# Optimization experiments

Hardware: AMD Instinct MI355X
Metric: run time of the kernel (lower is better)

Reference implementation:

```python
import jax, jax.numpy as jnp
import numpy as np

EMB_DIM = 1024
NUM_HEADS = 16
HEAD_DIM = EMB_DIM // NUM_HEADS
B, S = 4, 1024


def _split_heads(x):
    # [B, S, E] -> [B, H, S, E/H]
    b, s, e = x.shape
    return x.reshape(b, s, NUM_HEADS, e // NUM_HEADS).transpose(0, 2, 1, 3)


def _merge_heads(x):
    # [B, H, S, D] -> [B, S, H*D]
    b, h, s, d = x.shape
    return x.transpose(0, 2, 1, 3).reshape(b, s, h * d)


def setup_inputs() -> dict:
    key = jax.random.key(0)
    ks = jax.random.split(key, 8)
    w_scale = 0.02
    return {
        "Re": jax.random.normal(ks[0], (B, S, EMB_DIM), jnp.float32),
        "Im": jax.random.normal(ks[1], (B, S, EMB_DIM), jnp.float32),
        "pos_enc": jax.random.normal(ks[2], (B, S, HEAD_DIM), jnp.float32),
        "Wq": jax.random.normal(ks[3], (EMB_DIM, EMB_DIM), jnp.float32) * w_scale,
        "bq": jnp.zeros((EMB_DIM,), jnp.float32),
        "Wk": jax.random.normal(ks[4], (EMB_DIM, EMB_DIM), jnp.float32) * w_scale,
        "bk": jnp.zeros((EMB_DIM,), jnp.float32),
        "Wv": jax.random.normal(ks[5], (EMB_DIM, EMB_DIM), jnp.float32) * w_scale,
        "bv": jnp.zeros((EMB_DIM,), jnp.float32),
        "Wo": jax.random.normal(ks[6], (EMB_DIM, EMB_DIM), jnp.float32) * w_scale,
        "bo": jnp.zeros((EMB_DIM,), jnp.float32),
    }


def reference(Re, Im, pos_enc, Wq, bq, Wk, bk, Wv, bv, Wo, bo):
    # projections + head split
    Q = _split_heads(Re @ Wq + bq)          # [B,H,S,D]
    K = _split_heads(Re @ Wk + bk)          # [B,H,S,D]
    ImH = _split_heads(Im)                  # [B,H,S,D]
    P = pos_enc[:, None, :, :]              # [B,1,S,D] broadcast over heads
    Q = Q + P
    K = K + P
    # real part of (Q + i*Im)(K - i*Im)^T = Q K^T + Im Im^T
    denom = jnp.sqrt(jnp.asarray(EMB_DIM, Q.dtype))  # NOTE: sqrt(emb_dim), as in source
    scores = (jnp.einsum("bhqd,bhkd->bhqk", Q, K)
              + jnp.einsum("bhqd,bhkd->bhqk", ImH, ImH)) / denom
    weights = jax.nn.softmax(scores, axis=-1)
    V = _split_heads(Re @ Wv + bv) + P      # value_pos_enc=True
    out = jnp.einsum("bhqk,bhkd->bhqd", weights, V)
    return _merge_heads(out) @ Wo + bo
```

## Files before the change

kernel.cpp:

```cpp
#include <hip/hip_runtime.h>
#include <hip/hip_bf16.h>
#include <stdint.h>

#define BATCH 4
#define SEQ   1024
#define EMB   1024
#define NHEAD 16
#define HDIM  64
#define MTOT  (BATCH*SEQ)
#define MELEM (MTOT*EMB)

typedef __attribute__((ext_vector_type(8))) short short8;
typedef __attribute__((ext_vector_type(4))) float f32x4;
typedef __attribute__((ext_vector_type(16))) float f32x16;
typedef __attribute__((ext_vector_type(4))) unsigned short us4;
typedef __attribute__((ext_vector_type(2))) unsigned int u32x2;
typedef __attribute__((ext_vector_type(4))) unsigned int u32x4;

static __device__ __forceinline__ unsigned short f2bf_fast(float f) {
  unsigned u = __builtin_bit_cast(unsigned, f);
  return (unsigned short)((u + 0x8000u) >> 16);
}

static __device__ __forceinline__ unsigned cvt_pk_bf16(float lo, float hi) {
  unsigned r;
  asm("v_cvt_pk_bf16_f32 %0, %1, %2" : "=v"(r) : "v"(lo), "v"(hi));
  return r;
}

static __device__ __forceinline__ void cp16(const void* g, const void* lds_uniform) {
  __builtin_amdgcn_global_load_lds(
      (const __attribute__((address_space(1))) unsigned int*)(uintptr_t)g,
      (__attribute__((address_space(3))) unsigned int*)(unsigned int)(uintptr_t)lds_uniform,
      16, 0, 0);
}

__global__ __launch_bounds__(256) void cvt_bf16(const float* __restrict__ in0,
                                                const float* __restrict__ in1,
                                                short* __restrict__ out0,
                                                short* __restrict__ out1) {
  const float* in  = blockIdx.y ? in1  : in0;
  short*       out = blockIdx.y ? out1 : out0;
  int i = blockIdx.x * 256 + threadIdx.x;
  float4 f = ((const float4*)in)[i];
  unsigned r0 = ((unsigned)f2bf_fast(f.y) << 16) | f2bf_fast(f.x);
  unsigned r1 = ((unsigned)f2bf_fast(f.w) << 16) | f2bf_fast(f.z);
  ((uint2*)out)[i] = make_uint2(r0, r1);
}

__global__ __launch_bounds__(256) void wtrans(const float* __restrict__ W0,
                                              const float* __restrict__ W1,
                                              const float* __restrict__ W2,
                                              const float* __restrict__ W3,
                                              short* __restrict__ WtBase) {
  const int z = blockIdx.z;
  const float* W = (z == 0) ? W0 : (z == 1) ? W1 : (z == 2) ? W2 : W3;
  short* Wt = WtBase + (size_t)z * EMB * EMB;
  __shared__ short tile[32][33];
  int nT = blockIdx.x * 32, kT = blockIdx.y * 32;
  int tx = threadIdx.x, ty = threadIdx.y;
  #pragma unroll
  for (int i = 0; i < 4; ++i)
    tile[ty + 8*i][tx] = (short)f2bf_fast(W[(size_t)(kT + ty + 8*i) * EMB + nT + tx]);
  __syncthreads();
  #pragma unroll
  for (int i = 0; i < 4; ++i)
    Wt[(size_t)(nT + ty + 8*i) * EMB + kT + tx] = tile[tx][ty + 8*i];
}

__global__ __launch_bounds__(256) void gemm_qkv(const short* __restrict__ A,
                                                const short* __restrict__ Wt,
                                                const float* __restrict__ bq,
                                                const float* __restrict__ bk,
                                                const float* __restrict__ bv,
                                                const float* __restrict__ pos,
                                                short* __restrict__ QKbase,
                                                short* __restrict__ vtOut) {
  const int m0 = blockIdx.y * 128, n0 = blockIdx.x * 64;
  const int z = n0 >> 10;
  const float* bias = (z == 0) ? bq : (z == 1 ? bk : bv);

  __shared__ __align__(16) short As[128 * 64];
  __shared__ __align__(16) short Bs[64 * 64];

  const int t = threadIdx.x;
  const int lane = t & 63, w = t >> 6;
  const int wm = w >> 1, wn = w & 1;
  const int quad = lane >> 4, l16 = lane & 15;
  const int lrow8 = lane >> 3, lchunk = lane & 7;
  const int gch = lchunk ^ lrow8;
  const int sw7 = l16 & 7;

  const short* Arow = A  + (size_t)(m0 + w * 32 + lrow8) * EMB + gch * 8;
  const short* Brow = Wt + (size_t)(n0 + w * 16 + lrow8) * EMB + gch * 8;

  f32x4 acc[4][2] = {};

  for (int k0 = 0; k0 < EMB; k0 += 64) {
    #pragma unroll
    for (int s = 0; s < 4; ++s)
      cp16(Arow + (size_t)(s * 8) * EMB + k0, &As[(w * 32 + s * 8) * 64]);
    #pragma unroll
    for (int s = 0; s < 2; ++s)
      cp16(Brow + (size_t)(s * 8) * EMB + k0, &Bs[(w * 16 + s * 8) * 64]);
    __syncthreads();
    #pragma unroll
    for (int ks = 0; ks < 2; ++ks) {
      const int chv = ((ks << 2) + quad) ^ sw7;
      short8 af[4], bfr[2];
      #pragma unroll
      for (int i = 0; i < 4; ++i)
        af[i] = *(const short8*)&As[(wm * 64 + i * 16 + l16) * 64 + chv * 8];
      #pragma unroll
      for (int j = 0; j < 2; ++j)
        bfr[j] = *(const short8*)&Bs[(wn * 32 + j * 16 + l16) * 64 + chv * 8];
      #pragma unroll
      for (int i = 0; i < 4; ++i)
        #pragma unroll
        for (int j = 0; j < 2; ++j)
          acc[i][j] = __builtin_amdgcn_mfma_f32_16x16x32_bf16(af[i], bfr[j], acc[i][j], 0, 0, 0);
    }
    __syncthreads();
  }

  #pragma unroll
  for (int i = 0; i < 4; ++i) {
    int mbase = m0 + wm * 64 + i * 16 + quad * 4;
    #pragma unroll
    for (int j = 0; j < 2; ++j) {
      int n = n0 + wn * 32 + j * 16 + l16;
      int nl = n & 1023;
      float bn = bias[nl];
      int d = nl & (HDIM - 1);
      if (z == 2) {
        int bh = (mbase >> 10) * NHEAD + (nl >> 6);
        int s = mbase & (SEQ - 1);
        us4 pk;
        #pragma unroll
        for (int r = 0; r < 4; ++r) {
          float v = acc[i][j][r] + bn + pos[(size_t)(mbase + r) * HDIM + d];
          pk[r] = f2bf_fast(v);
        }
        *(us4*)&vtOut[((size_t)bh * HDIM + d) * SEQ + s] = pk;
      } else {
        #pragma unroll
        for (int r = 0; r < 4; ++r) {
          int mm = mbase + r;
          float v = acc[i][j][r] + bn + pos[(size_t)mm * HDIM + d];
          QKbase[(size_t)z * MELEM + (size_t)mm * EMB + nl] = (short)f2bf_fast(v);
        }
      }
    }
  }
}

__global__ __launch_bounds__(256) void gemm_wo(const short* __restrict__ A,
                                               const short* __restrict__ Bt,
                                               const float* __restrict__ bias,
                                               float* __restrict__ out) {
  const int m0 = blockIdx.y * 64, n0 = blockIdx.x * 64;

  __shared__ __align__(16) short As[64 * 64];
  __shared__ __align__(16) short Bs[64 * 64];

  const int t = threadIdx.x;
  const int lane = t & 63, w = t >> 6;
  const int wm = w >> 1, wn = w & 1;
  const int quad = lane >> 4, l16 = lane & 15;
  const int lrow8 = lane >> 3, lchunk = lane & 7;
  const int gch = lchunk ^ lrow8;
  const int sw7 = l16 & 7;

  const short* Arow = A  + (size_t)(m0 + w * 16 + lrow8) * EMB + gch * 8;
  const short* Brow = Bt + (size_t)(n0 + w * 16 + lrow8) * EMB + gch * 8;

  f32x4 acc[2][2] = {};

  for (int k0 = 0; k0 < EMB; k0 += 64) {
    #pragma unroll
    for (int s = 0; s < 2; ++s) {
      cp16(Arow + (size_t)(s * 8) * EMB + k0, &As[(w * 16 + s * 8) * 64]);
      cp16(Brow + (size_t)(s * 8) * EMB + k0, &Bs[(w * 16 + s * 8) * 64]);
    }
    __syncthreads();
    #pragma unroll
    for (int ks = 0; ks < 2; ++ks) {
      const int chv = ((ks << 2) + quad) ^ sw7;
      short8 af[2], bfr[2];
      #pragma unroll
      for (int i = 0; i < 2; ++i)
        af[i] = *(const short8*)&As[(wm * 32 + i * 16 + l16) * 64 + chv * 8];
      #pragma unroll
      for (int j = 0; j < 2; ++j)
        bfr[j] = *(const short8*)&Bs[(wn * 32 + j * 16 + l16) * 64 + chv * 8];
      #pragma unroll
      for (int i = 0; i < 2; ++i)
        #pragma unroll
        for (int j = 0; j < 2; ++j)
          acc[i][j] = __builtin_amdgcn_mfma_f32_16x16x32_bf16(af[i], bfr[j], acc[i][j], 0, 0, 0);
    }
    __syncthreads();
  }

  #pragma unroll
  for (int i = 0; i < 2; ++i) {
    int mbase = m0 + wm * 32 + i * 16 + quad * 4;
    #pragma unroll
    for (int j = 0; j < 2; ++j) {
      int n = n0 + wn * 32 + j * 16 + l16;
      float bn = bias[n];
      #pragma unroll
      for (int r = 0; r < 4; ++r)
        out[(size_t)(mbase + r) * EMB + n] = acc[i][j][r] + bn;
    }
  }
}

__global__ __launch_bounds__(256) void attn(const short* __restrict__ Qp,
                                            const short* __restrict__ Kp,
                                            const short* __restrict__ VtG,
                                            const short* __restrict__ Imb,
                                            short* __restrict__ attnA) {
  const int qb = blockIdx.y * 128;
  const int bh = blockIdx.x;
  const int b = bh >> 4, h = bh & 15;
  const int t = threadIdx.x, lane = t & 63, w = t >> 6;
  const int c31 = lane & 31;
  const int hi  = lane >> 5;
  const int lrow8 = lane >> 3, lchunk = lane & 7;
  const int gch = lchunk ^ lrow8;

  __shared__ __align__(16) short tiles[3 * 64 * 64];

  const int qrow = qb + w * 32 + c31;
  const size_t qbase = ((size_t)(b * SEQ + qrow)) * EMB + h * HDIM + hi * 8;
  short8 bq_[4], bim[4];
  #pragma unroll
  for (int ks = 0; ks < 4; ++ks) {
    bq_[ks] = *(const short8*)&Qp [qbase + ks * 16];
    bim[ks] = *(const short8*)&Imb[qbase + ks * 16];
  }

  float lrA = 0.f, lrB = 0.f;
  f32x16 o0 = {}, o1 = {};

  const float SC = 0.03125f * 1.44269504089f;
  const size_t kimBase = ((size_t)b * SEQ) * EMB + h * HDIM + gch * 8;
  const size_t vtBase  = ((size_t)bh * HDIM) * SEQ + gch * 8;

  #pragma unroll
  for (int s = 0; s < 6; ++s) {
    const int I = w * 6 + s;
    const int tz = I >> 3;
    const int row = ((I & 7) * 8) + lrow8;
    const short* g;
    if (tz == 0)      g = Kp  + kimBase + (size_t)row * EMB;
    else if (tz == 1) g = Imb + kimBase + (size_t)row * EMB;
    else              g = VtG + vtBase + (size_t)row * SEQ;
    cp16(g, &tiles[I * 512]);
  }
  __syncthreads();

  const int swz = c31 & 7;

  for (int kt = 0; kt < 16; ++kt) {
    const int kBaseN = (kt + 1) * 64;

    f32x16 s0 = {}, s1 = {};
    #pragma unroll
    for (int ks = 0; ks < 4; ++ks) {
      const int ch = ((ks * 2 + hi) ^ swz) * 8;
      const int r0off = c31 * 64 + ch, r1off = (32 + c31) * 64 + ch;
      short8 k0 = *(const short8*)&tiles[r0off];
      short8 k1 = *(const short8*)&tiles[r1off];
      short8 i0 = *(const short8*)&tiles[4096 + r0off];
      short8 i1 = *(const short8*)&tiles[4096 + r1off];
      s0 = __builtin_amdgcn_mfma_f32_32x32x16_bf16(k0, bq_[ks], s0, 0, 0, 0);
      s1 = __builtin_amdgcn_mfma_f32_32x32x16_bf16(k1, bq_[ks], s1, 0, 0, 0);
      s0 = __builtin_amdgcn_mfma_f32_32x32x16_bf16(i0, bim[ks], s0, 0, 0, 0);
      s1 = __builtin_amdgcn_mfma_f32_32x32x16_bf16(i1, bim[ks], s1, 0, 0, 0);
    }

    __syncthreads();

    if (kt != 15) {
      #pragma unroll
      for (int s = 0; s < 4; ++s) {
        const int I = w * 4 + s;
        const int row = ((I & 7) * 8) + lrow8;
        const short* g = ((I >> 3) ? Imb : Kp) + kimBase + (size_t)(kBaseN + row) * EMB;
        cp16(g, &tiles[I * 512]);
      }
    }

    float p0[16], p1[16];
    #pragma unroll
    for (int r = 0; r < 16; ++r) {
      p0[r] = __builtin_amdgcn_exp2f(s0[r] * SC);
      p1[r] = __builtin_amdgcn_exp2f(s1[r] * SC);
      lrA += p0[r];
      lrB += p1[r];
    }

    short8 ap[4];
    #pragma unroll
    for (int half = 0; half < 2; ++half) {
      {
        u32x2 sA = __builtin_amdgcn_permlane32_swap(
            cvt_pk_bf16(p0[half*8+0], p0[half*8+1]), cvt_pk_bf16(p0[half*8+4], p0[half*8+5]), false, false);
        u32x2 sB = __builtin_amdgcn_permlane32_swap(
            cvt_pk_bf16(p0[half*8+2], p0[half*8+3]), cvt_pk_bf16(p0[half*8+6], p0[half*8+7]), false, false);
        u32x4 wv = {sA[0], sB[0], sA[1], sB[1]};
        ap[half] = __builtin_bit_cast(short8, wv);
      }
      {
        u32x2 sA = __builtin_amdgcn_permlane32_swap(
            cvt_pk_bf16(p1[half*8+0], p1[half*8+1]), cvt_pk_bf16(p1[half*8+4], p1[half*8+5]), false, false);
        u32x2 sB = __builtin_amdgcn_permlane32_swap(
            cvt_pk_bf16(p1[half*8+2], p1[half*8+3]), cvt_pk_bf16(p1[half*8+6], p1[half*8+7]), false, false);
        u32x4 wv = {sA[0], sB[0], sA[1], sB[1]};
        ap[2 + half] = __builtin_bit_cast(short8, wv);
      }
    }

    #pragma unroll
    for (int ks = 0; ks < 4; ++ks) {
      const int ch = ((ks * 2 + hi) ^ swz) * 8;
      short8 v0 = *(const short8*)&tiles[8192 + c31 * 64 + ch];
      short8 v1 = *(const short8*)&tiles[8192 + (32 + c31) * 64 + ch];
      o0 = __builtin_amdgcn_mfma_f32_32x32x16_bf16(ap[ks], v0, o0, 0, 0, 0);
      o1 = __builtin_amdgcn_mfma_f32_32x32x16_bf16(ap[ks], v1, o1, 0, 0, 0);
    }

    __syncthreads();

    if (kt != 15) {
      #pragma unroll
      for (int s = 0; s < 2; ++s) {
        const int I = 16 + w * 2 + s;
        const int row = ((I & 7) * 8) + lrow8;
        cp16(VtG + vtBase + (size_t)row * SEQ + kBaseN, &tiles[I * 512]);
      }
    }
  }

  float lr = lrA + lrB;
  lr += __shfl_xor(lr, 32);
  float inv = 1.f / lr;

  #pragma unroll
  for (int r = 0; r < 16; ++r) {
    const int qr = (r & 3) + 8 * (r >> 2) + 4 * hi;
    const float invr = __shfl(inv, qr);
    const size_t base = ((size_t)(b * SEQ + qb + w * 32 + qr)) * EMB + h * HDIM + c31;
    attnA[base]      = (short)f2bf_fast(o0[r] * invr);
    attnA[base + 32] = (short)f2bf_fast(o1[r] * invr);
  }
}

extern "C" void kernel_launch(void* const* d_in, const int* in_sizes, int n_in,
                              void* d_out, int out_size, void* d_ws, size_t ws_size,
                              hipStream_t stream) {
  const float* Re  = (const float*)d_in[0];
  const float* Im  = (const float*)d_in[1];
  const float* pos = (const float*)d_in[2];
  const float* Wq  = (const float*)d_in[3];
  const float* bq  = (const float*)d_in[4];
  const float* Wk  = (const float*)d_in[5];
  const float* bk  = (const float*)d_in[6];
  const float* Wv  = (const float*)d_in[7];
  const float* bv  = (const float*)d_in[8];
  const float* Wo  = (const float*)d_in[9];
  const float* bo  = (const float*)d_in[10];

  short* ws    = (short*)d_ws;
  short* Rebf  = ws;
  short* Imbf  = ws + (size_t)MELEM;
  short* Wt    = ws + (size_t)2 * MELEM;
  short* Qp    = ws + (size_t)3 * MELEM;
  short* Kp    = Qp + (size_t)MELEM;
  short* VtG   = Qp + (size_t)2 * MELEM;
  short* attnA = ws + (size_t)6 * MELEM;

  cvt_bf16<<<dim3(MELEM / 1024, 2), 256, 0, stream>>>(Re, Im, Rebf, Imbf);

  wtrans<<<dim3(32, 32, 4), dim3(32, 8), 0, stream>>>(Wq, Wk, Wv, Wo, Wt);

  gemm_qkv<<<dim3(3 * EMB / 64, MTOT / 128), 256, 0, stream>>>(
      Rebf, Wt, bq, bk, bv, pos, Qp, VtG);

  attn<<<dim3(BATCH * NHEAD, SEQ / 128), 256, 0, stream>>>(
      Qp, Kp, VtG, Imbf, attnA);

  gemm_wo<<<dim3(EMB / 64, MTOT / 64), 256, 0, stream>>>(
      attnA, Wt + 3 * EMB * EMB, bo, (float*)d_out);
}
```

Before: 193.7 us.

## Double-buffer LDS tiles in projection GEMMs and merge prep kernels

Both the QKV and output-projection GEMMs now use two LDS buffers. The global-to-LDS copy of the next K-slice is issued before the MFMAs on the current slice, so load latency can overlap with compute. The bf16 conversion of Re/Im and the weight transposes are also merged into one kernel launch, removing one launch. The trade-off is double the LDS per block, which may lower occupancy in the larger QKV GEMM.

```diff
diff --git a/kernel.cpp b/kernel.cpp
--- a/kernel.cpp
+++ b/kernel.cpp
@@ -35,37 +35,41 @@
       16, 0, 0);
 }
 
-__global__ __launch_bounds__(256) void cvt_bf16(const float* __restrict__ in0,
-                                                const float* __restrict__ in1,
-                                                short* __restrict__ out0,
-                                                short* __restrict__ out1) {
-  const float* in  = blockIdx.y ? in1  : in0;
-  short*       out = blockIdx.y ? out1 : out0;
-  int i = blockIdx.x * 256 + threadIdx.x;
-  float4 f = ((const float4*)in)[i];
-  unsigned r0 = ((unsigned)f2bf_fast(f.y) << 16) | f2bf_fast(f.x);
-  unsigned r1 = ((unsigned)f2bf_fast(f.w) << 16) | f2bf_fast(f.z);
-  ((uint2*)out)[i] = make_uint2(r0, r1);
-}
-
-__global__ __launch_bounds__(256) void wtrans(const float* __restrict__ W0,
-                                              const float* __restrict__ W1,
-                                              const float* __restrict__ W2,
-                                              const float* __restrict__ W3,
-                                              short* __restrict__ WtBase) {
-  const int z = blockIdx.z;
-  const float* W = (z == 0) ? W0 : (z == 1) ? W1 : (z == 2) ? W2 : W3;
-  short* Wt = WtBase + (size_t)z * EMB * EMB;
+__global__ __launch_bounds__(256) void prep(const float* __restrict__ Re,
+                                            const float* __restrict__ Im,
+                                            short* __restrict__ Rebf,
+                                            short* __restrict__ Imbf,
+                                            const float* __restrict__ W0,
+                                            const float* __restrict__ W1,
+                                            const float* __restrict__ W2,
+                                            const float* __restrict__ W3,
+                                            short* __restrict__ WtBase) {
   __shared__ short tile[32][33];
-  int nT = blockIdx.x * 32, kT = blockIdx.y * 32;
-  int tx = threadIdx.x, ty = threadIdx.y;
-  #pragma unroll
-  for (int i = 0; i < 4; ++i)
-    tile[ty + 8*i][tx] = (short)f2bf_fast(W[(size_t)(kT + ty + 8*i) * EMB + nT + tx]);
-  __syncthreads();
-  #pragma unroll
-  for (int i = 0; i < 4; ++i)
-    Wt[(size_t)(nT + ty + 8*i) * EMB + kT + tx] = tile[tx][ty + 8*i];
+  const int bid = blockIdx.x;
+  if (bid < 8192) {
+    const float* in  = (bid >= 4096) ? Im   : Re;
+    short*       out = (bid >= 4096) ? Imbf : Rebf;
+    int i = (bid & 4095) * 256 + threadIdx.x;
+    float4 f = ((const float4*)in)[i];
+    unsigned r0 = ((unsigned)f2bf_fast(f.y) << 16) | f2bf_fast(f.x);
+    unsigned r1 = ((unsigned)f2bf_fast(f.w) << 16) | f2bf_fast(f.z);
+    ((uint2*)out)[i] = make_uint2(r0, r1);
+  } else {
+    const int wb = bid - 8192;
+    const int z = wb >> 10;
+    const float* W = (z == 0) ? W0 : (z == 1) ? W1 : (z == 2) ? W2 : W3;
+    short* Wt = WtBase + (size_t)z * EMB * EMB;
+    const int rem = wb & 1023;
+    const int nT = (rem & 31) * 32, kT = (rem >> 5) * 32;
+    const int tx = threadIdx.x & 31, ty = threadIdx.x >> 5;
+    #pragma unroll
+    for (int i = 0; i < 4; ++i)
+      tile[ty + 8*i][tx] = (short)f2bf_fast(W[(size_t)(kT + ty + 8*i) * EMB + nT + tx]);
+    __syncthreads();
+    #pragma unroll
+    for (int i = 0; i < 4; ++i)
+      Wt[(size_t)(nT + ty + 8*i) * EMB + kT + tx] = tile[tx][ty + 8*i];
+  }
 }
 
 __global__ __launch_bounds__(256) void gemm_qkv(const short* __restrict__ A,
@@ -80,8 +84,8 @@
   const int z = n0 >> 10;
   const float* bias = (z == 0) ? bq : (z == 1 ? bk : bv);
 
-  __shared__ __align__(16) short As[128 * 64];
-  __shared__ __align__(16) short Bs[64 * 64];
+  __shared__ __align__(16) short As[2][128 * 64];
+  __shared__ __align__(16) short Bs[2][64 * 64];
 
   const int t = threadIdx.x;
   const int lane = t & 63, w = t >> 6;
@@ -96,30 +100,43 @@
 
   f32x4 acc[4][2] = {};
 
-  for (int k0 = 0; k0 < EMB; k0 += 64) {
+  auto STAGE = [&](short* as, short* bs, int k0) {
     #pragma unroll
     for (int s = 0; s < 4; ++s)
-      cp16(Arow + (size_t)(s * 8) * EMB + k0, &As[(w * 32 + s * 8) * 64]);
+      cp16(Arow + (size_t)(s * 8) * EMB + k0, &as[(w * 32 + s * 8) * 64]);
     #pragma unroll
     for (int s = 0; s < 2; ++s)
-      cp16(Brow + (size_t)(s * 8) * EMB + k0, &Bs[(w * 16 + s * 8) * 64]);
-    __syncthreads();
+      cp16(Brow + (size_t)(s * 8) * EMB + k0, &bs[(w * 16 + s * 8) * 64]);
+  };
+  auto COMPUTE = [&](const short* as, const short* bs) {
     #pragma unroll
     for (int ks = 0; ks < 2; ++ks) {
       const int chv = ((ks << 2) + quad) ^ sw7;
       short8 af[4], bfr[2];
       #pragma unroll
       for (int i = 0; i < 4; ++i)
-        af[i] = *(const short8*)&As[(wm * 64 + i * 16 + l16) * 64 + chv * 8];
+        af[i] = *(const short8*)&as[(wm * 64 + i * 16 + l16) * 64 + chv * 8];
       #pragma unroll
       for (int j = 0; j < 2; ++j)
-        bfr[j] = *(const short8*)&Bs[(wn * 32 + j * 16 + l16) * 64 + chv * 8];
+        bfr[j] = *(const short8*)&bs[(wn * 32 + j * 16 + l16) * 64 + chv * 8];
       #pragma unroll
       for (int i = 0; i < 4; ++i)
         #pragma unroll
         for (int j = 0; j < 2; ++j)
           acc[i][j] = __builtin_amdgcn_mfma_f32_16x16x32_bf16(af[i], bfr[j], acc[i][j], 0, 0, 0);
     }
+  };
+
+  STAGE(As[0], Bs[0], 0);
+  __syncthreads();
+
+  for (int p = 0; p < 8; ++p) {
+    STAGE(As[1], Bs[1], p * 128 + 64);
+    COMPUTE(As[0], Bs[0]);
+    __syncthreads();
+    if (p != 7)
+      STAGE(As[0], Bs[0], p * 128 + 128);
+    COMPUTE(As[1], Bs[1]);
     __syncthreads();
   }
 
@@ -160,8 +177,8 @@
                                                float* __restrict__ out) {
   const int m0 = blockIdx.y * 64, n0 = blockIdx.x * 64;
 
-  __shared__ __align__(16) short As[64 * 64];
-  __shared__ __align__(16) short Bs[64 * 64];
+  __shared__ __align__(16) short As[2][64 * 64];
+  __shared__ __align__(16) short Bs[2][64 * 64];
 
   const int t = threadIdx.x;
   const int lane = t & 63, w = t >> 6;
@@ -176,29 +193,42 @@
 
   f32x4 acc[2][2] = {};
 
-  for (int k0 = 0; k0 < EMB; k0 += 64) {
+  auto STAGE = [&](short* as, short* bs, int k0) {
     #pragma unroll
     for (int s = 0; s < 2; ++s) {
-      cp16(Arow + (size_t)(s * 8) * EMB + k0, &As[(w * 16 + s * 8) * 64]);
-      cp16(Brow + (size_t)(s * 8) * EMB + k0, &Bs[(w * 16 + s * 8) * 64]);
-    }
-    __syncthreads();
+      cp16(Arow + (size_t)(s * 8) * EMB + k0, &as[(w * 16 + s * 8) * 64]);
+      cp16(Brow + (size_t)(s * 8) * EMB + k0, &bs[(w * 16 + s * 8) * 64]);
+    }
+  };
+  auto COMPUTE = [&](const short* as, const short* bs) {
     #pragma unroll
     for (int ks = 0; ks < 2; ++ks) {
       const int chv = ((ks << 2) + quad) ^ sw7;
       short8 af[2], bfr[2];
       #pragma unroll
       for (int i = 0; i < 2; ++i)
-        af[i] = *(const short8*)&As[(wm * 32 + i * 16 + l16) * 64 + chv * 8];
+        af[i] = *(const short8*)&as[(wm * 32 + i * 16 + l16) * 64 + chv * 8];
       #pragma unroll
       for (int j = 0; j < 2; ++j)
-        bfr[j] = *(const short8*)&Bs[(wn * 32 + j * 16 + l16) * 64 + chv * 8];
+        bfr[j] = *(const short8*)&bs[(wn * 32 + j * 16 + l16) * 64 + chv * 8];
       #pragma unroll
       for (int i = 0; i < 2; ++i)
         #pragma unroll
         for (int j = 0; j < 2; ++j)
           acc[i][j] = __builtin_amdgcn_mfma_f32_16x16x32_bf16(af[i], bfr[j], acc[i][j], 0, 0, 0);
     }
+  };
+
+  STAGE(As[0], Bs[0], 0);
+  __syncthreads();
+
+  for (int p = 0; p < 8; ++p) {
+    STAGE(As[1], Bs[1], p * 128 + 64);
+    COMPUTE(As[0], Bs[0]);
+    __syncthreads();
+    if (p != 7)
+      STAGE(As[0], Bs[0], p * 128 + 128);
+    COMPUTE(As[1], Bs[1]);
     __syncthreads();
   }
 
@@ -382,9 +412,7 @@
   short* VtG   = Qp + (size_t)2 * MELEM;
   short* attnA = ws + (size_t)6 * MELEM;
 
-  cvt_bf16<<<dim3(MELEM / 1024, 2), 256, 0, stream>>>(Re, Im, Rebf, Imbf);
-
-  wtrans<<<dim3(32, 32, 4), dim3(32, 8), 0, stream>>>(Wq, Wk, Wv, Wo, Wt);
+  prep<<<dim3(12288), 256, 0, stream>>>(Re, Im, Rebf, Imbf, Wq, Wk, Wv, Wo, Wt);
 
   gemm_qkv<<<dim3(3 * EMB / 64, MTOT / 128), 256, 0, stream>>>(
       Rebf, Wt, bq, bk, bv, pos, Qp, VtG);
```

Result: no change. 191.6 us (-1.1%).
